# Performance work log

Hardware: AMD Instinct MI355X
Metric: run time of the kernel (lower is better)

Reference implementation:

```python
import jax, jax.numpy as jnp
import numpy as np

IN_CH = 256
OUT_CH = 256
NUM_HEADS = 4
LOCAL_RADIUS = 2
SCALE = OUT_CH ** 0.5  # torch divides by out_channels**0.5


def setup_inputs() -> dict:
    key = jax.random.key(0)
    ks = jax.random.split(key, 7)
    B, C, H, W = 1, IN_CH, 48, 48
    x = jax.random.normal(ks[0], (B, C, H, W), dtype=jnp.float32)
    s = 0.02
    Wq = jax.random.normal(ks[1], (OUT_CH, IN_CH), dtype=jnp.float32) * s
    Wk = jax.random.normal(ks[2], (OUT_CH, IN_CH), dtype=jnp.float32) * s
    Wv = jax.random.normal(ks[3], (OUT_CH, IN_CH), dtype=jnp.float32) * s
    bq = jax.random.normal(ks[4], (OUT_CH,), dtype=jnp.float32) * s
    bk = jax.random.normal(ks[5], (OUT_CH,), dtype=jnp.float32) * s
    bv = jax.random.normal(ks[6], (OUT_CH,), dtype=jnp.float32) * s
    return {"x": x, "Wq": Wq, "bq": bq, "Wk": Wk, "bk": bk, "Wv": Wv, "bv": bv}


def reference(x, Wq, bq, Wk, bk, Wv, bv):
    B, C, H, W = x.shape
    N = H * W
    # Faithful to torch: x.view(B, N, -1) is a raw reshape of [B,C,H,W]
    xr = x.reshape(B, N, C)
    q = xr @ Wq.T + bq  # [B, N, OUT_CH]
    k = xr @ Wk.T + bk
    v = xr @ Wv.T + bv
    dh = OUT_CH // NUM_HEADS
    # [B, heads, N, dh]
    q = q.reshape(B, N, NUM_HEADS, dh).transpose(0, 2, 1, 3)
    k = k.reshape(B, N, NUM_HEADS, dh).transpose(0, 2, 1, 3)
    v = v.reshape(B, N, NUM_HEADS, dh).transpose(0, 2, 1, 3)
    acc = jnp.zeros_like(v)
    for h in range(-LOCAL_RADIUS, LOCAL_RADIUS + 1):
        for w in range(-LOCAL_RADIUS, LOCAL_RADIUS + 1):
            # torch rolls dims (-3, -2) of [B, heads, N, dh] -> axes (1, 2)
            rk = jnp.roll(k, shift=(h, w), axis=(1, 2))
            scores = jnp.einsum('bhnd,bhmd->bhnm', q, rk) / SCALE
            p = jax.nn.softmax(scores, axis=-1)  # dropout p=0 -> identity
            rv = jnp.roll(v, shift=(-h, -w), axis=(1, 2))
            acc = acc + jnp.einsum('bhnm,bhmd->bhnd', p, rv)
    out = acc.transpose(0, 2, 1, 3).reshape(B, N, NUM_HEADS * dh)
    return out
```

## Files before the change

### kernel.cpp

```cpp
#include <hip/hip_runtime.h>


#define N_TOK 2304
#define OUTC 256
#define HSZ (N_TOK * 64)

typedef _Float16 half8 __attribute__((ext_vector_type(8)));
typedef _Float16 half4 __attribute__((ext_vector_type(4)));
typedef float f32x4 __attribute__((ext_vector_type(4)));

typedef __attribute__((address_space(3))) unsigned int as3_u32;
typedef __attribute__((address_space(1))) unsigned int as1_u32;

__device__ __forceinline__ f32x4 mfma16(half8 a, half8 b, f32x4 c) {
  return __builtin_amdgcn_mfma_f32_16x16x32_f16(a, b, c, 0, 0, 0);
}

__device__ __forceinline__ void gload_lds16(const _Float16* g, _Float16* l) {
  __builtin_amdgcn_global_load_lds((const as1_u32*)g, (as3_u32*)l, 16, 0, 0);
}

__device__ __forceinline__ half8 cvt8(float4 a, float4 b) {
  half8 h;
  h[0] = (_Float16)a.x; h[1] = (_Float16)a.y; h[2] = (_Float16)a.z; h[3] = (_Float16)a.w;
  h[4] = (_Float16)b.x; h[5] = (_Float16)b.y; h[6] = (_Float16)b.z; h[7] = (_Float16)b.w;
  return h;
}

__global__ __launch_bounds__(256) void k_proj(
    const float* __restrict__ x, const float* __restrict__ Wq,
    const float* __restrict__ Wk, const float* __restrict__ Wv,
    const float* __restrict__ bq, const float* __restrict__ bk,
    const float* __restrict__ bv,
    _Float16* __restrict__ Qh, _Float16* __restrict__ KF, _Float16* __restrict__ VF) {
  __shared__ _Float16 stg[4096];
  const int w = threadIdx.x >> 6, lane = threadIdx.x & 63;
  const int lr = lane & 15, lk = lane >> 4;
  const int n0 = blockIdx.x * 64 + w * 16;
  const int o0 = blockIdx.y * 64;
  const int mat = blockIdx.z;
  const float* W = (mat == 0) ? Wq : (mat == 1) ? Wk : Wv;
  f32x4 acc[4] = {};

  if (mat == 2) {
    const float* rp0; const float* rp1; const float* rp2;
    const float* rp3; const float* rp4;
    {
      int r0 = (n0 + lr - 4 + N_TOK) % N_TOK;
      int r1 = (n0 + lr - 2 + N_TOK) % N_TOK;
      int r2 = (n0 + lr) % N_TOK;
      int r3 = (n0 + lr + 2) % N_TOK;
      int r4 = (n0 + lr + 4) % N_TOK;
      rp0 = x + (size_t)r0 * OUTC + 8 * lk;
      rp1 = x + (size_t)r1 * OUTC + 8 * lk;
      rp2 = x + (size_t)r2 * OUTC + 8 * lk;
      rp3 = x + (size_t)r3 * OUTC + 8 * lk;
      rp4 = x + (size_t)r4 * OUTC + 8 * lk;
    }
#pragma unroll
    for (int kk = 0; kk < 8; ++kk) {
      float4 s0 = *(const float4*)(rp0 + 32 * kk);
      float4 s1 = *(const float4*)(rp1 + 32 * kk);
      float4 s2 = *(const float4*)(rp2 + 32 * kk);
      float4 s3 = *(const float4*)(rp3 + 32 * kk);
      float4 s4 = *(const float4*)(rp4 + 32 * kk);
      float4 t0 = *(const float4*)(rp0 + 32 * kk + 4);
      float4 t1 = *(const float4*)(rp1 + 32 * kk + 4);
      float4 t2 = *(const float4*)(rp2 + 32 * kk + 4);
      float4 t3 = *(const float4*)(rp3 + 32 * kk + 4);
      float4 t4 = *(const float4*)(rp4 + 32 * kk + 4);
      float4 lo, hi;
      lo.x = s0.x + s1.x + s2.x + s3.x + s4.x;
      lo.y = s0.y + s1.y + s2.y + s3.y + s4.y;
      lo.z = s0.z + s1.z + s2.z + s3.z + s4.z;
      lo.w = s0.w + s1.w + s2.w + s3.w + s4.w;
      hi.x = t0.x + t1.x + t2.x + t3.x + t4.x;
      hi.y = t0.y + t1.y + t2.y + t3.y + t4.y;
      hi.z = t0.z + t1.z + t2.z + t3.z + t4.z;
      hi.w = t0.w + t1.w + t2.w + t3.w + t4.w;
      half8 a = cvt8(lo, hi);
#pragma unroll
      for (int c = 0; c < 4; ++c) {
        const float* wrow = W + (size_t)(o0 + 16*c + lr) * OUTC + 32*kk + 8*lk;
        half8 b = cvt8(*(const float4*)(wrow), *(const float4*)(wrow + 4));
        acc[c] = mfma16(a, b, acc[c]);
      }
    }
#pragma unroll
    for (int c = 0; c < 4; ++c) {
      float bo = 5.0f * bv[o0 + 16*c + lr];
#pragma unroll
      for (int r = 0; r < 4; ++r)
        stg[(c*128 + (w>>1)*64 + lk*16 + lr)*8 + 4*(w&1) + r] =
            (_Float16)(acc[c][r] + bo);
    }
    __syncthreads();
    _Float16* dst = VF + (size_t)blockIdx.y * HSZ + (size_t)blockIdx.x * 4096;
    ((half8*)dst)[threadIdx.x]       = ((const half8*)stg)[threadIdx.x];
    ((half8*)dst)[256 + threadIdx.x] = ((const half8*)stg)[256 + threadIdx.x];
    return;
  }

  const float* xrow = x + (size_t)(n0 + lr) * OUTC + 8 * lk;
#pragma unroll
  for (int kk = 0; kk < 8; ++kk) {
    half8 a = cvt8(*(const float4*)(xrow + 32 * kk),
                   *(const float4*)(xrow + 32 * kk + 4));
#pragma unroll
    for (int c = 0; c < 4; ++c) {
      const float* wrow = W + (size_t)(o0 + 16*c + lr) * OUTC + 32*kk + 8*lk;
      half8 b = cvt8(*(const float4*)(wrow), *(const float4*)(wrow + 4));
      acc[c] = mfma16(a, b, acc[c]);
    }
  }
  const float* bias = (mat == 0) ? bq : bk;
  const int hd = blockIdx.y;

  if (mat == 0) {
    const float qs = 0.0625f * 1.4426950408889634f;
#pragma unroll
    for (int c = 0; c < 4; ++c) {
      float bo = bias[o0 + 16*c + lr];
      int d = 16*c + lr;
#pragma unroll
      for (int r = 0; r < 4; ++r)
        stg[(w*16 + 4*lk + r) * 64 + d] = (_Float16)((acc[c][r] + bo) * qs);
    }
    __syncthreads();
    _Float16* dst = Qh + ((size_t)hd * N_TOK + blockIdx.x * 64) * 64;
    ((half8*)dst)[threadIdx.x]       = ((const half8*)stg)[threadIdx.x];
    ((half8*)dst)[256 + threadIdx.x] = ((const half8*)stg)[256 + threadIdx.x];
  } else {
#pragma unroll
    for (int c = 0; c < 4; ++c) {
      float bo = bias[o0 + 16*c + lr];
      int d = 16*c + lr;
      int h = d >> 5, g4K = (d >> 3) & 3, iiK = d & 7;
#pragma unroll
      for (int r = 0; r < 4; ++r)
        stg[(w*2 + h)*512 + (g4K*16 + 4*lk + r)*8 + iiK] = (_Float16)(acc[c][r] + bo);
    }
    __syncthreads();
    _Float16* dst = KF + (size_t)hd * HSZ + (size_t)blockIdx.x * 4096;
    ((half8*)dst)[threadIdx.x]       = ((const half8*)stg)[threadIdx.x];
    ((half8*)dst)[256 + threadIdx.x] = ((const half8*)stg)[256 + threadIdx.x];
  }
}

__global__ __launch_bounds__(256) void k_flash(
    const _Float16* __restrict__ Qh, const _Float16* __restrict__ KF,
    const _Float16* __restrict__ VF,
    _Float16* __restrict__ Opart, float* __restrict__ Lpart) {
  __shared__ __align__(16) _Float16 lds[2][8192];
  const int wv = threadIdx.x >> 6, lane = threadIdx.x & 63;
  const int lr = lane & 15, g4 = lane >> 4;
  const int strip = blockIdx.x * 4 + wv;
  const int n0 = strip * 32;
  const int pair = blockIdx.y;
  const int hd = pair >> 2, gk = pair & 3;
  const int chunk = blockIdx.z;
  const int vh = (2*hd + 4 - gk) & 3;

  const _Float16* Qp = Qh + ((size_t)hd * N_TOK + n0 + lr) * 64 + 8*g4;
  const half8 qa0 = *(const half8*)(Qp);
  const half8 qa1 = *(const half8*)(Qp + 32);
  const half8 qb0 = *(const half8*)(Qp + 16*64);
  const half8 qb1 = *(const half8*)(Qp + 16*64 + 32);

  const _Float16* Kt = KF + (size_t)gk * HSZ + (size_t)chunk * 9 * 4096;
  const _Float16* Vt = VF + (size_t)vh * HSZ + (size_t)chunk * 9 * 4096;
  const _Float16* gsrc = (wv < 2 ? Kt : Vt) + (wv & 1) * 2048 + lane * 8;
  const int ldsoff = (wv < 2 ? 0 : 4096) + (wv & 1) * 2048;

  f32x4 accA[4] = {}, accB[4] = {};
  f32x4 acclA = {}, acclB = {};
  half8 ones;
#pragma unroll
  for (int i = 0; i < 8; ++i) ones[i] = (_Float16)1.0f;

  auto stage = [&](int t, int b) {
    const _Float16* s = gsrc + (size_t)t * 4096;
    _Float16* d = &lds[b][ldsoff];
    gload_lds16(s,        d);
    gload_lds16(s + 512,  d + 512);
    gload_lds16(s + 1024, d + 1024);
    gload_lds16(s + 1536, d + 1536);
  };
  auto body = [&](int b) {
    const _Float16* ldsK = &lds[b][0]    + lane * 8;
    const _Float16* ldsV = &lds[b][4096] + lane * 8;
    f32x4 sA[4], sB[4];
    __builtin_amdgcn_s_setprio(1);
#pragma unroll
    for (int c = 0; c < 4; ++c) {
      half8 k0 = *(const half8*)(ldsK + c*1024);
      half8 k1 = *(const half8*)(ldsK + c*1024 + 512);
      f32x4 tA = {}; tA = mfma16(k0, qa0, tA); tA = mfma16(k1, qa1, tA); sA[c] = tA;
      f32x4 tB = {}; tB = mfma16(k0, qb0, tB); tB = mfma16(k1, qb1, tB); sB[c] = tB;
    }
    __builtin_amdgcn_s_setprio(0);
    half8 pa0, pa1, pb0, pb1;
#pragma unroll
    for (int c = 0; c < 4; ++c) {
      float eA0 = __builtin_amdgcn_exp2f(sA[c][0]);
      float eA1 = __builtin_amdgcn_exp2f(sA[c][1]);
      float eA2 = __builtin_amdgcn_exp2f(sA[c][2]);
      float eA3 = __builtin_amdgcn_exp2f(sA[c][3]);
      float eB0 = __builtin_amdgcn_exp2f(sB[c][0]);
      float eB1 = __builtin_amdgcn_exp2f(sB[c][1]);
      float eB2 = __builtin_amdgcn_exp2f(sB[c][2]);
      float eB3 = __builtin_amdgcn_exp2f(sB[c][3]);
      if (c == 0) {
        pa0[0]=(_Float16)eA0; pa0[1]=(_Float16)eA1; pa0[2]=(_Float16)eA2; pa0[3]=(_Float16)eA3;
        pb0[0]=(_Float16)eB0; pb0[1]=(_Float16)eB1; pb0[2]=(_Float16)eB2; pb0[3]=(_Float16)eB3;
      } else if (c == 1) {
        pa0[4]=(_Float16)eA0; pa0[5]=(_Float16)eA1; pa0[6]=(_Float16)eA2; pa0[7]=(_Float16)eA3;
        pb0[4]=(_Float16)eB0; pb0[5]=(_Float16)eB1; pb0[6]=(_Float16)eB2; pb0[7]=(_Float16)eB3;
      } else if (c == 2) {
        pa1[0]=(_Float16)eA0; pa1[1]=(_Float16)eA1; pa1[2]=(_Float16)eA2; pa1[3]=(_Float16)eA3;
        pb1[0]=(_Float16)eB0; pb1[1]=(_Float16)eB1; pb1[2]=(_Float16)eB2; pb1[3]=(_Float16)eB3;
      } else {
        pa1[4]=(_Float16)eA0; pa1[5]=(_Float16)eA1; pa1[6]=(_Float16)eA2; pa1[7]=(_Float16)eA3;
        pb1[4]=(_Float16)eB0; pb1[5]=(_Float16)eB1; pb1[6]=(_Float16)eB2; pb1[7]=(_Float16)eB3;
      }
    }
    __builtin_amdgcn_s_setprio(1);
#pragma unroll
    for (int cc = 0; cc < 4; ++cc) {
      half8 v0 = *(const half8*)(ldsV + cc*1024);
      half8 v1 = *(const half8*)(ldsV + cc*1024 + 512);
      accA[cc] = mfma16(v0, pa0, accA[cc]); accA[cc] = mfma16(v1, pa1, accA[cc]);
      accB[cc] = mfma16(v0, pb0, accB[cc]); accB[cc] = mfma16(v1, pb1, accB[cc]);
    }
    acclA = mfma16(ones, pa0, acclA); acclA = mfma16(ones, pa1, acclA);
    acclB = mfma16(ones, pb0, acclB); acclB = mfma16(ones, pb1, acclB);
    __builtin_amdgcn_s_setprio(0);
  };

  stage(0, 0);
#pragma unroll 1
  for (int t = 0; t < 9; ++t) {
    if (t < 8) {
      stage(t + 1, (t + 1) & 1);
      asm volatile("s_waitcnt vmcnt(4)" ::: "memory");
    } else {
      asm volatile("s_waitcnt vmcnt(0)" ::: "memory");
    }
    __builtin_amdgcn_sched_barrier(0);
    __builtin_amdgcn_s_barrier();
    __builtin_amdgcn_sched_barrier(0);
    body(t & 1);
    if (t < 8) {
      __builtin_amdgcn_sched_barrier(0);
      __builtin_amdgcn_s_barrier();
    }
  }

  float invA = 1.0f / acclA[0];
  float invB = 1.0f / acclB[0];
  _Float16* Oa = Opart + (((size_t)chunk * 16 + pair) * N_TOK + n0 + lr) * 64;
  _Float16* Ob = Oa + 16 * 64;
#pragma unroll
  for (int cc = 0; cc < 4; ++cc) {
    half4 ha, hb;
#pragma unroll
    for (int r = 0; r < 4; ++r) {
      ha[r] = (_Float16)(accA[cc][r] * invA);
      hb[r] = (_Float16)(accB[cc][r] * invB);
    }
    *(half4*)(Oa + 16*cc + 4*g4) = ha;
    *(half4*)(Ob + 16*cc + 4*g4) = hb;
  }
  if (g4 == 0) {
    Lpart[((size_t)chunk * 16 + pair) * N_TOK + n0 + lr] = acclA[0];
    Lpart[((size_t)chunk * 16 + pair) * N_TOK + n0 + 16 + lr] = acclB[0];
  }
}

__global__ __launch_bounds__(256) void k_combine(
    const _Float16* __restrict__ Opart, const float* __restrict__ Lpart,
    float* __restrict__ out) {
  int gid = blockIdx.x * 256 + threadIdx.x;
  int hd = gid / (N_TOK * 8);
  int rem = gid % (N_TOK * 8);
  int n = rem >> 3, db = (rem & 7) * 8;
  float acc[8] = {};
#pragma unroll
  for (int gk = 0; gk < 4; ++gk) {
    float cg = (((hd - gk) & 3) == 2) ? 2.0f : 1.0f;
    int pair = hd * 4 + gk;
    float la[4], lsum = 0.f;
#pragma unroll
    for (int ch = 0; ch < 4; ++ch) {
      la[ch] = Lpart[((size_t)ch * 16 + pair) * N_TOK + n];
      lsum += la[ch];
    }
    float rs = cg / lsum;
#pragma unroll
    for (int ch = 0; ch < 4; ++ch) {
      half8 v = *(const half8*)(Opart + (((size_t)ch * 16 + pair) * N_TOK + n) * 64 + db);
      float w = la[ch] * rs;
#pragma unroll
      for (int i = 0; i < 8; ++i) acc[i] += w * (float)v[i];
    }
  }
  float* dst = out + (size_t)n * OUTC + hd * 64 + db;
  float4 r0, r1;
  r0.x = acc[0]; r0.y = acc[1]; r0.z = acc[2]; r0.w = acc[3];
  r1.x = acc[4]; r1.y = acc[5]; r1.z = acc[6]; r1.w = acc[7];
  *(float4*)(dst)     = r0;
  *(float4*)(dst + 4) = r1;
}

extern "C" void kernel_launch(void* const* d_in, const int* in_sizes, int n_in,
                              void* d_out, int out_size, void* d_ws, size_t ws_size,
                              hipStream_t stream) {
  (void)in_sizes; (void)n_in; (void)out_size; (void)ws_size;
  const float* x  = (const float*)d_in[0];
  const float* Wq = (const float*)d_in[1];
  const float* bq = (const float*)d_in[2];
  const float* Wk = (const float*)d_in[3];
  const float* bk = (const float*)d_in[4];
  const float* Wv = (const float*)d_in[5];
  const float* bv = (const float*)d_in[6];

  char* ws = (char*)d_ws;
  float*    Lp  = (float*)   (ws);
  _Float16* Qh  = (_Float16*)(ws + 1179648);
  _Float16* KF  = (_Float16*)(ws + 2359296);
  _Float16* VF  = (_Float16*)(ws + 3538944);
  _Float16* Op  = (_Float16*)(ws + 4718592);
  float* out = (float*)d_out;

  k_proj   <<<dim3(36, 4, 3), dim3(256), 0, stream>>>(x, Wq, Wk, Wv, bq, bk, bv, Qh, KF, VF);
  k_flash  <<<dim3(18, 16, 4), dim3(256), 0, stream>>>(Qh, KF, VF, Op, Lp);
  k_combine<<<dim3(288), dim3(256), 0, stream>>>(Op, Lp, out);
}
```

Before: 69.61 us.

## Load V fragments directly into registers, keep only K in LDS

The flash kernel no longer stages V tiles through shared memory. Each wave now loads its V operand fragments straight from global memory into double-buffered registers, while K alone goes through a halved LDS double buffer that all four waves share. This removes the LDS round trip and bank traffic for V and cuts LDS use, which may allow more blocks per CU. In exchange each wave loads the full V tile redundantly (four times the global/L2 reads for V), register pressure rises by 16 half8 values, and the pipeline is restructured into a manually unrolled loop of two tiles per iteration with new vmcnt waits.

```diff
diff --git a/kernel.cpp b/kernel.cpp
--- a/kernel.cpp
+++ b/kernel.cpp
@@ -151,7 +151,7 @@
     const _Float16* __restrict__ Qh, const _Float16* __restrict__ KF,
     const _Float16* __restrict__ VF,
     _Float16* __restrict__ Opart, float* __restrict__ Lpart) {
-  __shared__ __align__(16) _Float16 lds[2][8192];
+  __shared__ __align__(16) _Float16 ldsK[2][4096];
   const int wv = threadIdx.x >> 6, lane = threadIdx.x & 63;
   const int lr = lane & 15, g4 = lane >> 4;
   const int strip = blockIdx.x * 4 + wv;
@@ -167,10 +167,9 @@
   const half8 qb0 = *(const half8*)(Qp + 16*64);
   const half8 qb1 = *(const half8*)(Qp + 16*64 + 32);
 
-  const _Float16* Kt = KF + (size_t)gk * HSZ + (size_t)chunk * 9 * 4096;
-  const _Float16* Vt = VF + (size_t)vh * HSZ + (size_t)chunk * 9 * 4096;
-  const _Float16* gsrc = (wv < 2 ? Kt : Vt) + (wv & 1) * 2048 + lane * 8;
-  const int ldsoff = (wv < 2 ? 0 : 4096) + (wv & 1) * 2048;
+  const _Float16* Ksrc = KF + (size_t)gk * HSZ + (size_t)chunk * 9 * 4096
+                         + wv * 1024 + lane * 8;
+  const _Float16* Vsrc = VF + (size_t)vh * HSZ + (size_t)chunk * 9 * 4096 + lane * 8;
 
   f32x4 accA[4] = {}, accB[4] = {};
   f32x4 acclA = {}, acclB = {};
@@ -178,23 +177,23 @@
 #pragma unroll
   for (int i = 0; i < 8; ++i) ones[i] = (_Float16)1.0f;
 
-  auto stage = [&](int t, int b) {
-    const _Float16* s = gsrc + (size_t)t * 4096;
-    _Float16* d = &lds[b][ldsoff];
-    gload_lds16(s,        d);
-    gload_lds16(s + 512,  d + 512);
-    gload_lds16(s + 1024, d + 1024);
-    gload_lds16(s + 1536, d + 1536);
+  auto stageK = [&](int t, int b) {
+    const _Float16* s = Ksrc + (size_t)t * 4096;
+    _Float16* d = &ldsK[b][wv * 1024];
+    gload_lds16(s, d);
+    gload_lds16(s + 512, d + 512);
   };
-  auto body = [&](int b) {
-    const _Float16* ldsK = &lds[b][0]    + lane * 8;
-    const _Float16* ldsV = &lds[b][4096] + lane * 8;
+
+  auto body = [&](const _Float16* ldsKbase,
+                  half8 v0, half8 v1, half8 v2, half8 v3,
+                  half8 v4, half8 v5, half8 v6, half8 v7) {
+    const _Float16* ldsKb = ldsKbase + lane * 8;
     f32x4 sA[4], sB[4];
     __builtin_amdgcn_s_setprio(1);
 #pragma unroll
     for (int c = 0; c < 4; ++c) {
-      half8 k0 = *(const half8*)(ldsK + c*1024);
-      half8 k1 = *(const half8*)(ldsK + c*1024 + 512);
+      half8 k0 = *(const half8*)(ldsKb + c*1024);
+      half8 k1 = *(const half8*)(ldsKb + c*1024 + 512);
       f32x4 tA = {}; tA = mfma16(k0, qa0, tA); tA = mfma16(k1, qa1, tA); sA[c] = tA;
       f32x4 tB = {}; tB = mfma16(k0, qb0, tB); tB = mfma16(k1, qb1, tB); sB[c] = tB;
     }
@@ -225,36 +224,57 @@
       }
     }
     __builtin_amdgcn_s_setprio(1);
-#pragma unroll
-    for (int cc = 0; cc < 4; ++cc) {
-      half8 v0 = *(const half8*)(ldsV + cc*1024);
-      half8 v1 = *(const half8*)(ldsV + cc*1024 + 512);
-      accA[cc] = mfma16(v0, pa0, accA[cc]); accA[cc] = mfma16(v1, pa1, accA[cc]);
-      accB[cc] = mfma16(v0, pb0, accB[cc]); accB[cc] = mfma16(v1, pb1, accB[cc]);
-    }
+    accA[0] = mfma16(v0, pa0, accA[0]); accA[0] = mfma16(v1, pa1, accA[0]);
+    accB[0] = mfma16(v0, pb0, accB[0]); accB[0] = mfma16(v1, pb1, accB[0]);
+    accA[1] = mfma16(v2, pa0, accA[1]); accA[1] = mfma16(v3, pa1, accA[1]);
+    accB[1] = mfma16(v2, pb0, accB[1]); accB[1] = mfma16(v3, pb1, accB[1]);
+    accA[2] = mfma16(v4, pa0, accA[2]); accA[2] = mfma16(v5, pa1, accA[2]);
+    accB[2] = mfma16(v4, pb0, accB[2]); accB[2] = mfma16(v5, pb1, accB[2]);
+    accA[3] = mfma16(v6, pa0, accA[3]); accA[3] = mfma16(v7, pa1, accA[3]);
+    accB[3] = mfma16(v6, pb0, accB[3]); accB[3] = mfma16(v7, pb1, accB[3]);
     acclA = mfma16(ones, pa0, acclA); acclA = mfma16(ones, pa1, acclA);
     acclB = mfma16(ones, pb0, acclB); acclB = mfma16(ones, pb1, acclB);
     __builtin_amdgcn_s_setprio(0);
   };
 
-  stage(0, 0);
+#define LOADV(B, t) do { const _Float16* vp_ = Vsrc + (size_t)(t) * 4096; \
+    B##0 = *(const half8*)(vp_);        B##1 = *(const half8*)(vp_ + 512); \
+    B##2 = *(const half8*)(vp_ + 1024); B##3 = *(const half8*)(vp_ + 1536); \
+    B##4 = *(const half8*)(vp_ + 2048); B##5 = *(const half8*)(vp_ + 2560); \
+    B##6 = *(const half8*)(vp_ + 3072); B##7 = *(const half8*)(vp_ + 3584); } while (0)
+
+  half8 vA0, vA1, vA2, vA3, vA4, vA5, vA6, vA7;
+  half8 vB0, vB1, vB2, vB3, vB4, vB5, vB6, vB7;
+
+  stageK(0, 0);
+  LOADV(vA, 0);
 #pragma unroll 1
-  for (int t = 0; t < 9; ++t) {
-    if (t < 8) {
-      stage(t + 1, (t + 1) & 1);
-      asm volatile("s_waitcnt vmcnt(4)" ::: "memory");
-    } else {
-      asm volatile("s_waitcnt vmcnt(0)" ::: "memory");
-    }
+  for (int u = 0; u < 4; ++u) {
+    const int t = 2 * u;
+    stageK(t + 1, 1);
+    LOADV(vB, t + 1);
+    asm volatile("s_waitcnt vmcnt(10)" ::: "memory");
     __builtin_amdgcn_sched_barrier(0);
     __builtin_amdgcn_s_barrier();
     __builtin_amdgcn_sched_barrier(0);
-    body(t & 1);
-    if (t < 8) {
-      __builtin_amdgcn_sched_barrier(0);
-      __builtin_amdgcn_s_barrier();
-    }
-  }
+    body(&ldsK[0][0], vA0, vA1, vA2, vA3, vA4, vA5, vA6, vA7);
+    __builtin_amdgcn_sched_barrier(0);
+    __builtin_amdgcn_s_barrier();
+    stageK(t + 2, 0);
+    LOADV(vA, t + 2);
+    asm volatile("s_waitcnt vmcnt(10)" ::: "memory");
+    __builtin_amdgcn_sched_barrier(0);
+    __builtin_amdgcn_s_barrier();
+    __builtin_amdgcn_sched_barrier(0);
+    body(&ldsK[1][0], vB0, vB1, vB2, vB3, vB4, vB5, vB6, vB7);
+    __builtin_amdgcn_sched_barrier(0);
+    __builtin_amdgcn_s_barrier();
+  }
+  asm volatile("s_waitcnt vmcnt(0)" ::: "memory");
+  __builtin_amdgcn_sched_barrier(0);
+  __builtin_amdgcn_s_barrier();
+  body(&ldsK[0][0], vA0, vA1, vA2, vA3, vA4, vA5, vA6, vA7);
+#undef LOADV
 
   float invA = 1.0f / acclA[0];
   float invB = 1.0f / acclB[0];
```

After: 74.96 us. 7.7% more time.
